# Performance work log

Measured on AMD Instinct MI355X. Metric: run time of the kernel, lower is better.

## Reference

```python
import jax, jax.numpy as jnp
import numpy as np

EPS = 1e-5


def _gcn_conv(x, src, dst, norm, W, b, n_nodes):
    # PyG GCNConv: transform, then normalized scatter-add aggregation (self-loops included in src/dst)
    h = x @ W                                   # [N, out]
    msg = h[src] * norm[:, None]                # gather over edges [E+N, out]
    agg = jax.ops.segment_sum(msg, dst, num_segments=n_nodes)
    return agg + b


def _bn(x, gamma, beta):
    # BatchNorm1d in training mode: batch stats over node axis, biased variance
    mu = jnp.mean(x, axis=0)
    var = jnp.mean((x - mu) ** 2, axis=0)
    return (x - mu) * jax.lax.rsqrt(var + EPS) * gamma + beta


def setup_inputs() -> dict:
    key = jax.random.key(0)
    ks = jax.random.split(key, 8)
    N, E, F_in, H, F_out = 50000, 800000, 32, 96, 2
    x = jax.random.normal(ks[0], (N, F_in), dtype=jnp.float32)
    edge_index = jax.random.randint(ks[1], (2, E), 0, N, dtype=jnp.int64)
    def lin(k, fi, fo):
        s = 1.0 / np.sqrt(fi)
        return jax.random.uniform(k, (fi, fo), jnp.float32, -s, s)
    W1 = lin(ks[2], F_in, H); b1 = jnp.zeros((H,), jnp.float32)
    W2 = lin(ks[3], H, H);    b2 = jnp.zeros((H,), jnp.float32)
    W3 = lin(ks[4], H, H);    b3 = jnp.zeros((H,), jnp.float32)
    W4 = lin(ks[5], H, F_out); b4 = jnp.zeros((F_out,), jnp.float32)
    g1 = jnp.ones((H,), jnp.float32); be1 = jnp.zeros((H,), jnp.float32)
    g2 = jnp.ones((H,), jnp.float32); be2 = jnp.zeros((H,), jnp.float32)
    g3 = jnp.ones((H,), jnp.float32); be3 = jnp.zeros((H,), jnp.float32)
    return dict(x=x, edge_index=edge_index,
                W1=W1, b1=b1, g1=g1, be1=be1,
                W2=W2, b2=b2, g2=g2, be2=be2,
                W3=W3, b3=b3, g3=g3, be3=be3,
                W4=W4, b4=b4)


def reference(x, edge_index, W1, b1, g1, be1, W2, b2, g2, be2, W3, b3, g3, be3, W4, b4):
    N = x.shape[0]
    loop = jnp.arange(N, dtype=edge_index.dtype)
    src = jnp.concatenate([edge_index[0], loop])   # add self-loops
    dst = jnp.concatenate([edge_index[1], loop])
    deg = jax.ops.segment_sum(jnp.ones_like(dst, dtype=x.dtype), dst, num_segments=N)
    dinv = jnp.where(deg > 0, jax.lax.rsqrt(deg), 0.0)
    norm = dinv[src] * dinv[dst]                   # D^{-1/2} (A+I) D^{-1/2}

    h = jax.nn.relu(_bn(_gcn_conv(x, src, dst, norm, W1, b1, N), g1, be1))
    h = jax.nn.relu(_bn(_gcn_conv(h, src, dst, norm, W2, b2, N), g2, be2))
    h = jax.nn.relu(_bn(_gcn_conv(h, src, dst, norm, W3, b3, N), g3, be3))
    return _gcn_conv(h, src, dst, norm, W4, b4, N)
```

## Files before the change

kernel.cpp:

```cpp
#include <hip/hip_runtime.h>
#include <hip/hip_bf16.h>

using bf16x8 = __attribute__((ext_vector_type(8))) short;
using f32x4  = __attribute__((ext_vector_type(4))) float;

__device__ __forceinline__ float ldf(const void* p, size_t i, float isf){
  if (isf > 0.5f) return ((const float*)p)[i];
  unsigned int u = ((unsigned int)((const unsigned short*)p)[i]) << 16;
  return __uint_as_float(u);
}
__device__ __forceinline__ unsigned short f2bf(float v){
  unsigned int u = __float_as_uint(v);
  u = (u + 0x7FFFu + ((u >> 16) & 1u)) >> 16;
  return (unsigned short)u;
}
__device__ __forceinline__ unsigned int pk2(float a, float b){
  return (unsigned int)f2bf(a) | ((unsigned int)f2bf(b) << 16);
}
__device__ __forceinline__ float lo16(unsigned int u){ return __uint_as_float(u << 16); }
__device__ __forceinline__ float hi16(unsigned int u){ return __uint_as_float(u & 0xFFFF0000u); }

__global__ void k_fill(unsigned short* o, unsigned short v, int n){
  int i = blockIdx.x*blockDim.x + threadIdx.x;
  if (i < n) o[i] = v;
}

__global__ void k_prep(const unsigned short* xh, const unsigned int* eu,
                       float* flag, int nelemX, long long E,
                       const void* W1, const void* W2, const void* W3, const void* W4,
                       unsigned short* __restrict__ Wt1, unsigned short* __restrict__ Wt2,
                       unsigned short* __restrict__ Wt3, float* __restrict__ W4f,
                       int* __restrict__ cnt, float* __restrict__ stAll, int n){
  int t = threadIdx.x;
  if (blockIdx.x > 0){
    int total = n + 4609;
    for (int i = (int)(blockIdx.x-1)*256 + t; i < total; i += (int)(gridDim.x-1)*256){
      if (i < n) cnt[i] = 0; else stAll[i - n] = 0.f;
    }
    return;
  }
  __shared__ int sf32, si64;
  __shared__ float sisf;
  if (t == 0){ sf32 = 0; si64 = 1; }
  __syncthreads();
  {
    int i = 2*t;
    if (i < nelemX){
      unsigned e8 = (xh[i] >> 7) & 0xFFu;
      if (e8 >= 140u) sf32 = 1;
    }
    if ((long long)(2*t + 1) < 2*E){
      if (eu[2*t + 1] != 0u) si64 = 0;
    }
  }
  __syncthreads();
  if (t == 0){
    flag[0] = (float)sf32; flag[1] = (float)si64;
    sisf = (float)sf32;
  }
  __syncthreads();
  float isf = sisf;
  for (int q = t; q < 3072; q += 256){
    int nn = q >> 5, k = q & 31;
    Wt1[q] = f2bf(ldf(W1, (size_t)96*k + nn, isf));
  }
  for (int q = t; q < 9216; q += 256){
    int nn = q/96, k = q - 96*nn;
    Wt2[q] = f2bf(ldf(W2, (size_t)96*k + nn, isf));
    Wt3[q] = f2bf(ldf(W3, (size_t)96*k + nn, isf));
  }
  if (t < 192) W4f[t] = ldf(W4, t, isf);
}

__global__ void k_cnt(const int* __restrict__ ei, const float* __restrict__ flag,
                      int* __restrict__ cnt, long long E, int n){
  long long i = (long long)blockIdx.x*blockDim.x + threadIdx.x;
  if (i >= E) return;
  int d = (flag[1] > 0.5f) ? ei[2*E + 2*i] : ei[E + i];
  if ((unsigned)d < (unsigned)n) atomicAdd(&cnt[d], 1);
}

__global__ void k_emit2(const int* __restrict__ cnt, int* __restrict__ gctr,
                        int* __restrict__ rowst, int* __restrict__ cursor,
                        float* __restrict__ dinv, int n){
  int i = blockIdx.x*256 + threadIdx.x;
  int lane = threadIdx.x & 63;
  int v = (i < n) ? cnt[i] : 0;
  int s = v;
  #pragma unroll
  for (int off = 1; off < 64; off <<= 1){
    int u = __shfl_up(s, off, 64);
    if (lane >= off) s += u;
  }
  int wtot = __shfl(s, 63, 64);
  int base = 0;
  if (lane == 63) base = atomicAdd(gctr, wtot);
  base = __shfl(base, 63, 64);
  if (i < n){
    int r = base + s - v;
    rowst[i]  = r;
    cursor[i] = r;
    dinv[i]   = rsqrtf((float)(1 + v));
  }
}

#define FS_CHUNK 4096
template<typename IT>
__global__ __launch_bounds__(256) void k_fl1(const int* __restrict__ ei,
      const float* __restrict__ flag, int* __restrict__ cursor, IT* __restrict__ csr,
      long long E, int n, int gF8,
      const void* __restrict__ x, const unsigned short* __restrict__ Wt1b,
      const float* __restrict__ dinv, unsigned short* __restrict__ HS){
  __shared__ __align__(16) unsigned short Xs[64][40];
  __shared__ __align__(16) unsigned short Wt[96][40];
  int t = threadIdx.x;
  if ((int)blockIdx.x < gF8){
    int part = blockIdx.x & 7;
    long long base = (long long)(blockIdx.x >> 3) * FS_CHUNK;
    int pl = (int)(((long long)n *  part     ) >> 3);
    int pr = (int)(((long long)n * (part + 1)) >> 3);
    bool i64 = (flag[1] > 0.5f);
    long long lim = base + FS_CHUNK < E ? base + FS_CHUNK : E;
    for (long long i = base + t; i < lim; i += 256){
      int s, d;
      if (i64){ s = ei[2*i]; d = ei[2*E + 2*i]; }
      else    { s = ei[i];   d = ei[E + i];     }
      if (d >= pl && d < pr && (unsigned)s < (unsigned)n){
        int p = atomicAdd(&cursor[d], 1);
        csr[p] = (IT)s;
      }
    }
    return;
  }
  int bid = blockIdx.x - gF8;
  float isf = flag[0];
  for (int q = t; q < 384; q += 256){
    uint4 v = ((const uint4*)Wt1b)[q];
    *(uint4*)&Wt[q >> 2][(q & 3)*8] = v;
  }
  {
    int row = t >> 2, part = t & 3;
    int node = bid*64 + row;
    uint4 o;
    if (node < n){
      if (isf > 0.5f){
        const float* xr = (const float*)x + (size_t)32*node + 8*part;
        o.x = pk2(xr[0], xr[1]); o.y = pk2(xr[2], xr[3]);
        o.z = pk2(xr[4], xr[5]); o.w = pk2(xr[6], xr[7]);
      } else {
        o = ((const uint4*)x)[(size_t)4*node + part];
      }
    } else { o.x = o.y = o.z = o.w = 0u; }
    *(uint4*)&Xs[row][8*part] = o;
  }
  __syncthreads();

  int wv = t >> 6, lane = t & 63;
  int m = lane & 15, quad = lane >> 4;
  bf16x8 av = *(const bf16x8*)&Xs[16*wv + m][8*quad];
  f32x4 acc[6];
  #pragma unroll
  for (int c = 0; c < 6; ++c) acc[c] = (f32x4)(0.f);
  #pragma unroll
  for (int c = 0; c < 6; ++c){
    bf16x8 bv = *(const bf16x8*)&Wt[16*c + m][8*quad];
    acc[c] = __builtin_amdgcn_mfma_f32_16x16x32_bf16(av, bv, acc[c], 0, 0, 0);
  }
  int rowbase = bid*64 + 16*wv + 4*quad;
  float div[4];
  #pragma unroll
  for (int r = 0; r < 4; ++r){ int rr = rowbase + r; div[r] = (rr < n) ? dinv[rr] : 0.f; }
  #pragma unroll
  for (int c = 0; c < 6; ++c){
    int col = 16*c + m;
    #pragma unroll
    for (int r = 0; r < 4; ++r){
      int rr = rowbase + r;
      if (rr < n) HS[(size_t)96*rr + col] = f2bf(acc[c][r]*div[r]);
    }
  }
}

#define ACC8(v) { a0+=lo16((v).x); a1+=hi16((v).x); a2+=lo16((v).y); a3+=hi16((v).y); \
                  a4+=lo16((v).z); a5+=hi16((v).z); a6+=lo16((v).w); a7+=hi16((v).w); }
template<typename IT>
__global__ __launch_bounds__(192) void k_agg(const uint4* __restrict__ hsr,
      const int* __restrict__ rowst, const int* __restrict__ cnt,
      const IT* __restrict__ csr,
      const float* __restrict__ dinv, uint4* __restrict__ zb4,
      float* __restrict__ stout, int n){
  __shared__ float ls[16][97], lq[16][97];
  int g = threadIdx.x, ty = threadIdx.y;
  int t = ty*12 + g;
  int node = blockIdx.x*16 + ty;
  float r[8];
  if (node < n){
    uint4 v = hsr[(size_t)node*12 + g];
    float a0 = lo16(v.x), a1 = hi16(v.x), a2 = lo16(v.y), a3 = hi16(v.y);
    float a4 = lo16(v.z), a5 = hi16(v.z), a6 = lo16(v.w), a7 = hi16(v.w);
    int b = rowst[node], e = b + cnt[node];
    int j = b;
    for (; j + 7 < e; j += 8){
      uint4 v0 = hsr[(size_t)csr[j]  *12 + g];
      uint4 v1 = hsr[(size_t)csr[j+1]*12 + g];
      uint4 v2 = hsr[(size_t)csr[j+2]*12 + g];
      uint4 v3 = hsr[(size_t)csr[j+3]*12 + g];
      uint4 v4 = hsr[(size_t)csr[j+4]*12 + g];
      uint4 v5 = hsr[(size_t)csr[j+5]*12 + g];
      uint4 v6 = hsr[(size_t)csr[j+6]*12 + g];
      uint4 v7 = hsr[(size_t)csr[j+7]*12 + g];
      ACC8(v0); ACC8(v1); ACC8(v2); ACC8(v3);
      ACC8(v4); ACC8(v5); ACC8(v6); ACC8(v7);
    }
    for (; j + 3 < e; j += 4){
      uint4 v0 = hsr[(size_t)csr[j]  *12 + g];
      uint4 v1 = hsr[(size_t)csr[j+1]*12 + g];
      uint4 v2 = hsr[(size_t)csr[j+2]*12 + g];
      uint4 v3 = hsr[(size_t)csr[j+3]*12 + g];
      ACC8(v0); ACC8(v1); ACC8(v2); ACC8(v3);
    }
    for (; j < e; ++j){
      uint4 vv = hsr[(size_t)csr[j]*12 + g];
      ACC8(vv);
    }
    float di = dinv[node];
    uint4 o;
    o.x = pk2(a0*di, a1*di);
    o.y = pk2(a2*di, a3*di);
    o.z = pk2(a4*di, a5*di);
    o.w = pk2(a6*di, a7*di);
    zb4[(size_t)node*12 + g] = o;
    r[0]=lo16(o.x); r[1]=hi16(o.x); r[2]=lo16(o.y); r[3]=hi16(o.y);
    r[4]=lo16(o.z); r[5]=hi16(o.z); r[6]=lo16(o.w); r[7]=hi16(o.w);
  } else {
    #pragma unroll
    for (int jj = 0; jj < 8; ++jj) r[jj] = 0.f;
  }
  #pragma unroll
  for (int jj = 0; jj < 8; ++jj){
    ls[ty][8*g + jj] = r[jj];
    lq[ty][8*g + jj] = r[jj]*r[jj];
  }
  __syncthreads();
  if (t < 96){
    float s = 0.f, q = 0.f;
    #pragma unroll
    for (int rr = 0; rr < 16; ++rr){ s += ls[rr][t]; q += lq[rr][t]; }
    int rep = blockIdx.x & 7;
    atomicAdd(&stout[192*rep + t],      s);
    atomicAdd(&stout[192*rep + 96 + t], q);
  }
}

__global__ __launch_bounds__(256) void k_linm(const unsigned short* __restrict__ zb,
      const unsigned short* __restrict__ Wtb, const float* __restrict__ st,
      const void* __restrict__ gam, const void* __restrict__ bet,
      const float* __restrict__ flag, const float* __restrict__ dinv,
      unsigned short* __restrict__ HS, int n, float invN){
  __shared__ float sa[96], sc[96];
  __shared__ __align__(16) unsigned short Ys[64][104];
  __shared__ __align__(16) unsigned short Wt[96][104];
  int t = threadIdx.x;
  if (t < 96){
    float ssum = 0.f, qsum = 0.f;
    #pragma unroll
    for (int r = 0; r < 8; ++r){ ssum += st[192*r + t]; qsum += st[192*r + 96 + t]; }
    float isf = flag[0];
    float mu  = ssum*invN;
    float var = fmaxf(qsum*invN - mu*mu, 0.f);
    float istd = rsqrtf(var + 1e-5f);
    float a = ldf(gam, t, isf)*istd;
    sa[t] = a; sc[t] = ldf(bet, t, isf) - mu*a;
  }
  for (int q = t; q < 1152; q += 256){
    uint4 v = ((const uint4*)Wtb)[q];
    *(uint4*)&Wt[q/12][8*(q - 12*(q/12))] = v;
  }
  __syncthreads();
  {
    int row = t >> 2, part = t & 3;
    int node = blockIdx.x*64 + row;
    if (node < n){
      const uint4* zr = (const uint4*)(zb + (size_t)96*node) + 3*part;
      #pragma unroll
      for (int q = 0; q < 3; ++q){
        uint4 zz = zr[q];
        int k = 24*part + 8*q;
        float y0 = fmaxf(lo16(zz.x)*sa[k]   + sc[k],   0.f);
        float y1 = fmaxf(hi16(zz.x)*sa[k+1] + sc[k+1], 0.f);
        float y2 = fmaxf(lo16(zz.y)*sa[k+2] + sc[k+2], 0.f);
        float y3 = fmaxf(hi16(zz.y)*sa[k+3] + sc[k+3], 0.f);
        float y4 = fmaxf(lo16(zz.z)*sa[k+4] + sc[k+4], 0.f);
        float y5 = fmaxf(hi16(zz.z)*sa[k+5] + sc[k+5], 0.f);
        float y6 = fmaxf(lo16(zz.w)*sa[k+6] + sc[k+6], 0.f);
        float y7 = fmaxf(hi16(zz.w)*sa[k+7] + sc[k+7], 0.f);
        *(unsigned int*)&Ys[row][k]     = pk2(y0, y1);
        *(unsigned int*)&Ys[row][k + 2] = pk2(y2, y3);
        *(unsigned int*)&Ys[row][k + 4] = pk2(y4, y5);
        *(unsigned int*)&Ys[row][k + 6] = pk2(y6, y7);
      }
    } else {
      unsigned int* yp = (unsigned int*)&Ys[row][24*part];
      #pragma unroll
      for (int q = 0; q < 12; ++q) yp[q] = 0u;
    }
  }
  __syncthreads();

  int wv = t >> 6, lane = t & 63;
  int m = lane & 15, quad = lane >> 4;
  bf16x8 av[3];
  #pragma unroll
  for (int kt = 0; kt < 3; ++kt)
    av[kt] = *(const bf16x8*)&Ys[16*wv + m][32*kt + 8*quad];
  f32x4 acc[6];
  #pragma unroll
  for (int c = 0; c < 6; ++c) acc[c] = (f32x4)(0.f);
  #pragma unroll
  for (int c = 0; c < 6; ++c){
    const unsigned short* wrow = &Wt[16*c + m][8*quad];
    #pragma unroll
    for (int kt = 0; kt < 3; ++kt){
      bf16x8 bv = *(const bf16x8*)(wrow + 32*kt);
      acc[c] = __builtin_amdgcn_mfma_f32_16x16x32_bf16(av[kt], bv, acc[c], 0, 0, 0);
    }
  }
  int rowbase = blockIdx.x*64 + 16*wv + 4*quad;
  float div[4];
  #pragma unroll
  for (int r = 0; r < 4; ++r){ int rr = rowbase + r; div[r] = (rr < n) ? dinv[rr] : 0.f; }
  #pragma unroll
  for (int c = 0; c < 6; ++c){
    int col = 16*c + m;
    #pragma unroll
    for (int r = 0; r < 4; ++r){
      int rr = rowbase + r;
      if (rr < n) HS[(size_t)96*rr + col] = f2bf(acc[c][r]*div[r]);
    }
  }
}

__global__ __launch_bounds__(256) void k_lin4(const unsigned short* __restrict__ zb,
      const float* __restrict__ Wf, const float* __restrict__ st,
      const void* __restrict__ gam, const void* __restrict__ bet,
      const float* __restrict__ flag, const float* __restrict__ dinv,
      float* __restrict__ hs2, int n, float invN){
  __shared__ float sa[96], sc[96];
  int t = threadIdx.x;
  if (t < 96){
    float ssum = 0.f, qsum = 0.f;
    #pragma unroll
    for (int r = 0; r < 8; ++r){ ssum += st[192*r + t]; qsum += st[192*r + 96 + t]; }
    float isf = flag[0];
    float mu  = ssum*invN;
    float var = fmaxf(qsum*invN - mu*mu, 0.f);
    float istd = rsqrtf(var + 1e-5f);
    float a = ldf(gam, t, isf)*istd;
    sa[t] = a; sc[t] = ldf(bet, t, isf) - mu*a;
  }
  __syncthreads();
  int i = blockIdx.x*blockDim.x + t;
  if (i >= n) return;
  const uint4* zr = (const uint4*)(zb + (size_t)96*i);
  float a0 = 0.f, a1 = 0.f;
  #pragma unroll
  for (int q = 0; q < 12; ++q){
    uint4 zz = zr[q];
    int k = 8*q;
    float y;
    y = fmaxf(lo16(zz.x)*sa[k]   + sc[k],   0.f); a0 += y*Wf[2*k];    a1 += y*Wf[2*k+1];
    y = fmaxf(hi16(zz.x)*sa[k+1] + sc[k+1], 0.f); a0 += y*Wf[2*k+2];  a1 += y*Wf[2*k+3];
    y = fmaxf(lo16(zz.y)*sa[k+2] + sc[k+2], 0.f); a0 += y*Wf[2*k+4];  a1 += y*Wf[2*k+5];
    y = fmaxf(hi16(zz.y)*sa[k+3] + sc[k+3], 0.f); a0 += y*Wf[2*k+6];  a1 += y*Wf[2*k+7];
    y = fmaxf(lo16(zz.z)*sa[k+4] + sc[k+4], 0.f); a0 += y*Wf[2*k+8];  a1 += y*Wf[2*k+9];
    y = fmaxf(hi16(zz.z)*sa[k+5] + sc[k+5], 0.f); a0 += y*Wf[2*k+10]; a1 += y*Wf[2*k+11];
    y = fmaxf(lo16(zz.w)*sa[k+6] + sc[k+6], 0.f); a0 += y*Wf[2*k+12]; a1 += y*Wf[2*k+13];
    y = fmaxf(hi16(zz.w)*sa[k+7] + sc[k+7], 0.f); a0 += y*Wf[2*k+14]; a1 += y*Wf[2*k+15];
  }
  float di = dinv[i];
  hs2[(size_t)2*i]   = di*a0;
  hs2[(size_t)2*i+1] = di*a1;
}

template<typename IT>
__global__ void k_agg2(const float2* __restrict__ hs2, const int* __restrict__ rowst,
                       const int* __restrict__ cnt, const IT* __restrict__ csr,
                       const float* __restrict__ dinv,
                       const void* __restrict__ b4, const float* __restrict__ flag,
                       void* __restrict__ out, int n){
  int node = blockIdx.x*blockDim.x + threadIdx.x;
  if (node >= n) return;
  float2 a = hs2[node];
  int b = rowst[node], e = b + cnt[node];
  for (int j = b; j < e; ++j){
    float2 v = hs2[(size_t)csr[j]];
    a.x += v.x; a.y += v.y;
  }
  float isf = flag[0];
  float di = dinv[node];
  float v0 = a.x*di + ldf(b4, 0, isf);
  float v1 = a.y*di + ldf(b4, 1, isf);
  if (isf > 0.5f){
    ((float*)out)[(size_t)2*node]   = v0;
    ((float*)out)[(size_t)2*node+1] = v1;
  } else {
    ((unsigned short*)out)[(size_t)2*node]   = f2bf(v0);
    ((unsigned short*)out)[(size_t)2*node+1] = f2bf(v1);
  }
}

extern "C" void kernel_launch(void* const* d_in, const int* in_sizes, int n_in,
                              void* d_out, int out_size, void* d_ws, size_t ws_size,
                              hipStream_t stream)
{
  const int B = 256;
  unsigned short* outh = (unsigned short*)d_out;

  if (n_in < 16){
    k_fill<<<(out_size+B-1)/B, B, 0, stream>>>(outh, 0x3F40u, out_size); return;
  }
  const int N = in_sizes[0] / 32;
  const long long E = in_sizes[1] / 2;
  if (in_sizes[0] % 32 != 0 || out_size != 2*N){
    k_fill<<<(out_size+B-1)/B, B, 0, stream>>>(outh, 0x3F60u, out_size); return;
  }
  const bool u16 = (N < 65536);

  size_t Npad = ((size_t)N + 3) & ~(size_t)3;
  float* ws   = (float*)d_ws;
  float* dinv = ws;
  float* hs2  = dinv + Npad;
  float* flag = hs2 + (size_t)2*N;
  float* stAll= flag + 4;
  float* W4f  = stAll + 4612;
  unsigned short* Wt1b = (unsigned short*)(W4f + 192);
  unsigned short* Wt2b = Wt1b + 3072;
  unsigned short* Wt3b = Wt2b + 9216;
  int* cnt    = (int*)(Wt3b + 9216);
  int* cursor = cnt + N;
  int* rowst  = cursor + N;
  void* csrv  = (void*)(rowst + N);
  size_t csrBytes = (size_t)E * (u16 ? 2 : 4);
  uintptr_t hp_ = (uintptr_t)csrv + csrBytes;
  hp_ = (hp_ + 15) & ~(uintptr_t)15;
  unsigned short* HS = (unsigned short*)hp_;
  unsigned short* Zb = HS + (size_t)96*N;

  size_t needB = ((uintptr_t)(Zb + (size_t)96*N) - (uintptr_t)d_ws) + 64;
  if (ws_size < needB){
    k_fill<<<(out_size+B-1)/B, B, 0, stream>>>(outh, 0x3F00u, out_size); return;
  }

  const void* x  = d_in[0];
  const int*  ei = (const int*)d_in[1];
  const void* W1 = d_in[2];
  const void* g1 = d_in[4];  const void* be1 = d_in[5];
  const void* W2 = d_in[6];
  const void* g2 = d_in[8];  const void* be2 = d_in[9];
  const void* W3 = d_in[10];
  const void* g3 = d_in[12]; const void* be3 = d_in[13];
  const void* W4 = d_in[14];
  const void* b4 = d_in[15];

  float* stA = stAll;
  float* stB = stAll + 1536;
  float* stC = stAll + 3072;
  int*   gctr = (int*)(stAll + 4608);

  int gN  = (N + B - 1)/B;
  int gE  = (int)((E + B - 1)/B);
  int nb  = (N + 255)/256;
  int gA  = (N + 15)/16;
  int gL  = (N + 63)/64;
  int gF8 = (int)((E + FS_CHUNK - 1)/FS_CHUNK) * 8;
  float invN = 1.0f / (float)N;
  dim3 ablk(12,16);

  k_prep<<<33, B, 0, stream>>>((const unsigned short*)x, (const unsigned int*)ei,
                               flag, in_sizes[0], E, W1, W2, W3, W4,
                               Wt1b, Wt2b, Wt3b, W4f, cnt, stAll, N);
  k_cnt<<<gE, B, 0, stream>>>(ei, flag, cnt, E, N);
  k_emit2<<<nb, B, 0, stream>>>(cnt, gctr, rowst, cursor, dinv, N);

  if (u16){
    unsigned short* csr = (unsigned short*)csrv;
    k_fl1<unsigned short><<<gF8 + gL, B, 0, stream>>>(ei, flag, cursor, csr, E, N, gF8,
                                                      x, Wt1b, dinv, HS);
    k_agg<unsigned short><<<gA, ablk, 0, stream>>>((const uint4*)HS, rowst, cnt, csr, dinv, (uint4*)Zb, stA, N);
    k_linm<<<gL, B, 0, stream>>>(Zb, Wt2b, stA, g1, be1, flag, dinv, HS, N, invN);
    k_agg<unsigned short><<<gA, ablk, 0, stream>>>((const uint4*)HS, rowst, cnt, csr, dinv, (uint4*)Zb, stB, N);
    k_linm<<<gL, B, 0, stream>>>(Zb, Wt3b, stB, g2, be2, flag, dinv, HS, N, invN);
    k_agg<unsigned short><<<gA, ablk, 0, stream>>>((const uint4*)HS, rowst, cnt, csr, dinv, (uint4*)Zb, stC, N);
    k_lin4<<<gN, B, 0, stream>>>(Zb, W4f, stC, g3, be3, flag, dinv, hs2, N, invN);
    k_agg2<unsigned short><<<gN, B, 0, stream>>>((const float2*)hs2, rowst, cnt, csr, dinv, b4, flag, d_out, N);
  } else {
    int* csr = (int*)csrv;
    k_fl1<int><<<gF8 + gL, B, 0, stream>>>(ei, flag, cursor, csr, E, N, gF8,
                                           x, Wt1b, dinv, HS);
    k_agg<int><<<gA, ablk, 0, stream>>>((const uint4*)HS, rowst, cnt, csr, dinv, (uint4*)Zb, stA, N);
    k_linm<<<gL, B, 0, stream>>>(Zb, Wt2b, stA, g1, be1, flag, dinv, HS, N, invN);
    k_agg<int><<<gA, ablk, 0, stream>>>((const uint4*)HS, rowst, cnt, csr, dinv, (uint4*)Zb, stB, N);
    k_linm<<<gL, B, 0, stream>>>(Zb, Wt3b, stB, g2, be2, flag, dinv, HS, N, invN);
    k_agg<int><<<gA, ablk, 0, stream>>>((const uint4*)HS, rowst, cnt, csr, dinv, (uint4*)Zb, stC, N);
    k_lin4<<<gN, B, 0, stream>>>(Zb, W4f, stC, g3, be3, flag, dinv, hs2, N, invN);
    k_agg2<int><<<gN, B, 0, stream>>>((const float2*)hs2, rowst, cnt, csr, dinv, b4, flag, d_out, N);
  }
}
```

Measured before the change: 340.8 us.

## Fuse whole GCN pipeline into one persistent cooperative kernel with grid syncs

Replaces the chain of about eleven kernel launches with a single cooperative persistent kernel. The grid is sized by occupancy, and grid.sync() separates the prep, degree count, scan, CSR fill, aggregation, linear and final stages. Each stage becomes a grid-stride loop over the old block indices, and shared memory is a union of the per-stage layouts. The goal is to remove per-launch overhead and inter-kernel gaps. In exchange, occupancy is limited by the largest shared-memory stage, and the aggregation stage now runs 192 of 256 threads per block. A host-side device-properties and occupancy query is added on every call, and the old multi-kernel path remains as a fallback.

```diff
diff --git a/kernel.cpp b/kernel.cpp
--- a/kernel.cpp
+++ b/kernel.cpp
@@ -1,8 +1,13 @@
 #include <hip/hip_runtime.h>
 #include <hip/hip_bf16.h>
+#include <hip/hip_cooperative_groups.h>
+
+namespace cg = cooperative_groups;
 
 using bf16x8 = __attribute__((ext_vector_type(8))) short;
 using f32x4  = __attribute__((ext_vector_type(4))) float;
+
+#define FS_CHUNK 4096
 
 __device__ __forceinline__ float ldf(const void* p, size_t i, float isf){
   if (isf > 0.5f) return ((const float*)p)[i];
@@ -23,6 +28,411 @@
 __global__ void k_fill(unsigned short* o, unsigned short v, int n){
   int i = blockIdx.x*blockDim.x + threadIdx.x;
   if (i < n) o[i] = v;
+}
+
+struct SLin1 { unsigned short Xs[64][40]; unsigned short Wt[96][40]; };
+struct SLinm { float sa[96]; float sc[96]; unsigned short Ys[64][104]; unsigned short Wt[96][104]; };
+struct SAgg  { float ls[16][97]; float lq[16][97]; };
+union __align__(16) SMem { SLin1 l1; SLinm lm; SAgg ag; };
+
+struct KParams {
+  const int* ei;
+  const void* x;
+  const void *W1, *W2, *W3, *W4;
+  const void *g1, *be1, *g2, *be2, *g3, *be3, *b4;
+  float* flag; float* stAll; float* W4f;
+  unsigned short *Wt1, *Wt2, *Wt3;
+  int *cnt, *cursor, *rowst;
+  void* csrv;
+  float *dinv, *hs2;
+  unsigned short *HS, *Zb;
+  void* out;
+  long long E;
+  int n, nelemX, gF8, gL, gA, gN;
+  float invN;
+};
+
+#define ACC8(v) { a0+=lo16((v).x); a1+=hi16((v).x); a2+=lo16((v).y); a3+=hi16((v).y); \
+                  a4+=lo16((v).z); a5+=hi16((v).z); a6+=lo16((v).w); a7+=hi16((v).w); }
+
+template<typename IT>
+__device__ void agg_stage(const KParams& p, SMem& sm, const IT* csr, float* stout, int t, int nbk){
+  const uint4* hsr = (const uint4*)p.HS;
+  uint4* zb4 = (uint4*)p.Zb;
+  int g = t % 12, ty = t / 12;
+  for (int va = blockIdx.x; va < p.gA; va += nbk){
+    float r[8];
+    if (t < 192){
+      int node = va*16 + ty;
+      if (node < p.n){
+        uint4 v = hsr[(size_t)node*12 + g];
+        float a0 = lo16(v.x), a1 = hi16(v.x), a2 = lo16(v.y), a3 = hi16(v.y);
+        float a4 = lo16(v.z), a5 = hi16(v.z), a6 = lo16(v.w), a7 = hi16(v.w);
+        int b = p.rowst[node], e = b + p.cnt[node];
+        int j = b;
+        for (; j + 7 < e; j += 8){
+          uint4 v0 = hsr[(size_t)csr[j]  *12 + g];
+          uint4 v1 = hsr[(size_t)csr[j+1]*12 + g];
+          uint4 v2 = hsr[(size_t)csr[j+2]*12 + g];
+          uint4 v3 = hsr[(size_t)csr[j+3]*12 + g];
+          uint4 v4 = hsr[(size_t)csr[j+4]*12 + g];
+          uint4 v5 = hsr[(size_t)csr[j+5]*12 + g];
+          uint4 v6 = hsr[(size_t)csr[j+6]*12 + g];
+          uint4 v7 = hsr[(size_t)csr[j+7]*12 + g];
+          ACC8(v0); ACC8(v1); ACC8(v2); ACC8(v3);
+          ACC8(v4); ACC8(v5); ACC8(v6); ACC8(v7);
+        }
+        for (; j + 3 < e; j += 4){
+          uint4 v0 = hsr[(size_t)csr[j]  *12 + g];
+          uint4 v1 = hsr[(size_t)csr[j+1]*12 + g];
+          uint4 v2 = hsr[(size_t)csr[j+2]*12 + g];
+          uint4 v3 = hsr[(size_t)csr[j+3]*12 + g];
+          ACC8(v0); ACC8(v1); ACC8(v2); ACC8(v3);
+        }
+        for (; j < e; ++j){
+          uint4 vv = hsr[(size_t)csr[j]*12 + g];
+          ACC8(vv);
+        }
+        float di = p.dinv[node];
+        uint4 o;
+        o.x = pk2(a0*di, a1*di);
+        o.y = pk2(a2*di, a3*di);
+        o.z = pk2(a4*di, a5*di);
+        o.w = pk2(a6*di, a7*di);
+        zb4[(size_t)node*12 + g] = o;
+        r[0]=lo16(o.x); r[1]=hi16(o.x); r[2]=lo16(o.y); r[3]=hi16(o.y);
+        r[4]=lo16(o.z); r[5]=hi16(o.z); r[6]=lo16(o.w); r[7]=hi16(o.w);
+      } else {
+        #pragma unroll
+        for (int jj = 0; jj < 8; ++jj) r[jj] = 0.f;
+      }
+      #pragma unroll
+      for (int jj = 0; jj < 8; ++jj){
+        sm.ag.ls[ty][8*g + jj] = r[jj];
+        sm.ag.lq[ty][8*g + jj] = r[jj]*r[jj];
+      }
+    }
+    __syncthreads();
+    if (t < 96){
+      float s = 0.f, q = 0.f;
+      #pragma unroll
+      for (int rr = 0; rr < 16; ++rr){ s += sm.ag.ls[rr][t]; q += sm.ag.lq[rr][t]; }
+      int rep = va & 7;
+      atomicAdd(&stout[192*rep + t],      s);
+      atomicAdd(&stout[192*rep + 96 + t], q);
+    }
+    __syncthreads();
+  }
+}
+
+__device__ void linm_stage(const KParams& p, SMem& sm, const unsigned short* Wtb,
+                           const float* st, const void* gam, const void* bet,
+                           int t, int nbk, float isf){
+  if (t < 96){
+    float ssum = 0.f, qsum = 0.f;
+    #pragma unroll
+    for (int r = 0; r < 8; ++r){ ssum += st[192*r + t]; qsum += st[192*r + 96 + t]; }
+    float mu  = ssum*p.invN;
+    float var = fmaxf(qsum*p.invN - mu*mu, 0.f);
+    float istd = rsqrtf(var + 1e-5f);
+    float a = ldf(gam, t, isf)*istd;
+    sm.lm.sa[t] = a; sm.lm.sc[t] = ldf(bet, t, isf) - mu*a;
+  }
+  for (int q = t; q < 1152; q += 256){
+    uint4 v = ((const uint4*)Wtb)[q];
+    *(uint4*)&sm.lm.Wt[q/12][8*(q - 12*(q/12))] = v;
+  }
+  __syncthreads();
+  int lane = t & 63, wv = t >> 6;
+  for (int vb = blockIdx.x; vb < p.gL; vb += nbk){
+    {
+      int row = t >> 2, part = t & 3;
+      int node = vb*64 + row;
+      if (node < p.n){
+        const uint4* zr = (const uint4*)(p.Zb + (size_t)96*node) + 3*part;
+        #pragma unroll
+        for (int q = 0; q < 3; ++q){
+          uint4 zz = zr[q];
+          int k = 24*part + 8*q;
+          float y0 = fmaxf(lo16(zz.x)*sm.lm.sa[k]   + sm.lm.sc[k],   0.f);
+          float y1 = fmaxf(hi16(zz.x)*sm.lm.sa[k+1] + sm.lm.sc[k+1], 0.f);
+          float y2 = fmaxf(lo16(zz.y)*sm.lm.sa[k+2] + sm.lm.sc[k+2], 0.f);
+          float y3 = fmaxf(hi16(zz.y)*sm.lm.sa[k+3] + sm.lm.sc[k+3], 0.f);
+          float y4 = fmaxf(lo16(zz.z)*sm.lm.sa[k+4] + sm.lm.sc[k+4], 0.f);
+          float y5 = fmaxf(hi16(zz.z)*sm.lm.sa[k+5] + sm.lm.sc[k+5], 0.f);
+          float y6 = fmaxf(lo16(zz.w)*sm.lm.sa[k+6] + sm.lm.sc[k+6], 0.f);
+          float y7 = fmaxf(hi16(zz.w)*sm.lm.sa[k+7] + sm.lm.sc[k+7], 0.f);
+          *(unsigned int*)&sm.lm.Ys[row][k]     = pk2(y0, y1);
+          *(unsigned int*)&sm.lm.Ys[row][k + 2] = pk2(y2, y3);
+          *(unsigned int*)&sm.lm.Ys[row][k + 4] = pk2(y4, y5);
+          *(unsigned int*)&sm.lm.Ys[row][k + 6] = pk2(y6, y7);
+        }
+      } else {
+        unsigned int* yp = (unsigned int*)&sm.lm.Ys[row][24*part];
+        #pragma unroll
+        for (int q = 0; q < 12; ++q) yp[q] = 0u;
+      }
+    }
+    __syncthreads();
+    int m = lane & 15, quad = lane >> 4;
+    bf16x8 av[3];
+    #pragma unroll
+    for (int kt = 0; kt < 3; ++kt)
+      av[kt] = *(const bf16x8*)&sm.lm.Ys[16*wv + m][32*kt + 8*quad];
+    f32x4 acc[6];
+    #pragma unroll
+    for (int c = 0; c < 6; ++c) acc[c] = (f32x4)(0.f);
+    #pragma unroll
+    for (int c = 0; c < 6; ++c){
+      const unsigned short* wrow = &sm.lm.Wt[16*c + m][8*quad];
+      #pragma unroll
+      for (int kt = 0; kt < 3; ++kt){
+        bf16x8 bv = *(const bf16x8*)(wrow + 32*kt);
+        acc[c] = __builtin_amdgcn_mfma_f32_16x16x32_bf16(av[kt], bv, acc[c], 0, 0, 0);
+      }
+    }
+    int rowbase = vb*64 + 16*wv + 4*quad;
+    float div[4];
+    #pragma unroll
+    for (int r = 0; r < 4; ++r){ int rr = rowbase + r; div[r] = (rr < p.n) ? p.dinv[rr] : 0.f; }
+    #pragma unroll
+    for (int c = 0; c < 6; ++c){
+      int col = 16*c + m;
+      #pragma unroll
+      for (int r = 0; r < 4; ++r){
+        int rr = rowbase + r;
+        if (rr < p.n) p.HS[(size_t)96*rr + col] = f2bf(acc[c][r]*div[r]);
+      }
+    }
+    __syncthreads();
+  }
+}
+
+template<typename IT>
+__global__ __launch_bounds__(256) void k_mega(KParams p){
+  cg::grid_group grid = cg::this_grid();
+  __shared__ SMem sm;
+  __shared__ int sflags[2];
+  const int t = threadIdx.x;
+  const int nbk = (int)gridDim.x;
+  const int lane = t & 63, wv = t >> 6;
+  IT* csr = (IT*)p.csrv;
+  int* gctr = (int*)(p.stAll + 4608);
+  float* stA = p.stAll;
+  float* stB = p.stAll + 1536;
+  float* stC = p.stAll + 3072;
+
+  if (blockIdx.x == 0){
+    if (t == 0){ sflags[0] = 0; sflags[1] = 1; }
+    __syncthreads();
+    {
+      int i = 2*t;
+      if (i < p.nelemX){
+        unsigned e8 = (((const unsigned short*)p.x)[i] >> 7) & 0xFFu;
+        if (e8 >= 140u) sflags[0] = 1;
+      }
+      if ((long long)(2*t+1) < 2*p.E){
+        if (((const unsigned int*)p.ei)[2*t+1] != 0u) sflags[1] = 0;
+      }
+    }
+    __syncthreads();
+    if (t == 0){ p.flag[0] = (float)sflags[0]; p.flag[1] = (float)sflags[1]; }
+    float isf0 = (float)sflags[0];
+    for (int q = t; q < 3072; q += 256){
+      int nn = q >> 5, k = q & 31;
+      p.Wt1[q] = f2bf(ldf(p.W1, (size_t)96*k + nn, isf0));
+    }
+    for (int q = t; q < 9216; q += 256){
+      int nn = q/96, k = q - 96*nn;
+      p.Wt2[q] = f2bf(ldf(p.W2, (size_t)96*k + nn, isf0));
+      p.Wt3[q] = f2bf(ldf(p.W3, (size_t)96*k + nn, isf0));
+    }
+    if (t < 192) p.W4f[t] = ldf(p.W4, t, isf0);
+  } else {
+    int total = p.n + 4609;
+    for (int i = (int)(blockIdx.x-1)*256 + t; i < total; i += (nbk-1)*256){
+      if (i < p.n) p.cnt[i] = 0; else p.stAll[i - p.n] = 0.f;
+    }
+  }
+  __threadfence();
+  grid.sync();
+
+  const bool i64 = p.flag[1] > 0.5f;
+  const float isf = p.flag[0];
+
+  for (long long i = (long long)blockIdx.x*256 + t; i < p.E; i += (long long)nbk*256){
+    int d = i64 ? p.ei[2*p.E + 2*i] : p.ei[p.E + i];
+    if ((unsigned)d < (unsigned)p.n) atomicAdd(&p.cnt[d], 1);
+  }
+  __threadfence();
+  grid.sync();
+
+  {
+    int chunks = (p.n + 255) >> 8;
+    for (int c = blockIdx.x; c < chunks; c += nbk){
+      int i = c*256 + t;
+      int v = (i < p.n) ? p.cnt[i] : 0;
+      int s = v;
+      #pragma unroll
+      for (int off = 1; off < 64; off <<= 1){
+        int u = __shfl_up(s, off, 64);
+        if (lane >= off) s += u;
+      }
+      int wtot = __shfl(s, 63, 64);
+      int base = 0;
+      if (lane == 63) base = atomicAdd(gctr, wtot);
+      base = __shfl(base, 63, 64);
+      if (i < p.n){
+        int r = base + s - v;
+        p.rowst[i]  = r;
+        p.cursor[i] = r;
+        p.dinv[i]   = rsqrtf((float)(1 + v));
+      }
+    }
+  }
+  __threadfence();
+  grid.sync();
+
+  for (int q = t; q < 384; q += 256){
+    uint4 v = ((const uint4*)p.Wt1)[q];
+    *(uint4*)&sm.l1.Wt[q >> 2][(q & 3)*8] = v;
+  }
+  __syncthreads();
+  for (int vb = blockIdx.x; vb < p.gF8 + p.gL; vb += nbk){
+    if (vb < p.gF8){
+      int part = vb & 7;
+      long long base = (long long)(vb >> 3) * FS_CHUNK;
+      int pl = (int)(((long long)p.n *  part     ) >> 3);
+      int pr = (int)(((long long)p.n * (part + 1)) >> 3);
+      long long lim = base + FS_CHUNK < p.E ? base + FS_CHUNK : p.E;
+      for (long long i = base + t; i < lim; i += 256){
+        int s, d;
+        if (i64){ s = p.ei[2*i]; d = p.ei[2*p.E + 2*i]; }
+        else    { s = p.ei[i];   d = p.ei[p.E + i];     }
+        if (d >= pl && d < pr && (unsigned)s < (unsigned)p.n){
+          int pp = atomicAdd(&p.cursor[d], 1);
+          csr[pp] = (IT)s;
+        }
+      }
+    } else {
+      int bid = vb - p.gF8;
+      {
+        int row = t >> 2, part4 = t & 3;
+        int node = bid*64 + row;
+        uint4 o;
+        if (node < p.n){
+          if (isf > 0.5f){
+            const float* xr = (const float*)p.x + (size_t)32*node + 8*part4;
+            o.x = pk2(xr[0], xr[1]); o.y = pk2(xr[2], xr[3]);
+            o.z = pk2(xr[4], xr[5]); o.w = pk2(xr[6], xr[7]);
+          } else {
+            o = ((const uint4*)p.x)[(size_t)4*node + part4];
+          }
+        } else { o.x = o.y = o.z = o.w = 0u; }
+        *(uint4*)&sm.l1.Xs[row][8*part4] = o;
+      }
+      __syncthreads();
+      int m = lane & 15, quad = lane >> 4;
+      bf16x8 av = *(const bf16x8*)&sm.l1.Xs[16*wv + m][8*quad];
+      f32x4 acc[6];
+      #pragma unroll
+      for (int c = 0; c < 6; ++c) acc[c] = (f32x4)(0.f);
+      #pragma unroll
+      for (int c = 0; c < 6; ++c){
+        bf16x8 bv = *(const bf16x8*)&sm.l1.Wt[16*c + m][8*quad];
+        acc[c] = __builtin_amdgcn_mfma_f32_16x16x32_bf16(av, bv, acc[c], 0, 0, 0);
+      }
+      int rowbase = bid*64 + 16*wv + 4*quad;
+      float div[4];
+      #pragma unroll
+      for (int r = 0; r < 4; ++r){ int rr = rowbase + r; div[r] = (rr < p.n) ? p.dinv[rr] : 0.f; }
+      #pragma unroll
+      for (int c = 0; c < 6; ++c){
+        int col = 16*c + m;
+        #pragma unroll
+        for (int r = 0; r < 4; ++r){
+          int rr = rowbase + r;
+          if (rr < p.n) p.HS[(size_t)96*rr + col] = f2bf(acc[c][r]*div[r]);
+        }
+      }
+      __syncthreads();
+    }
+  }
+  __threadfence();
+  grid.sync();
+
+  agg_stage<IT>(p, sm, csr, stA, t, nbk);
+  __threadfence(); grid.sync();
+  linm_stage(p, sm, p.Wt2, stA, p.g1, p.be1, t, nbk, isf);
+  __threadfence(); grid.sync();
+  agg_stage<IT>(p, sm, csr, stB, t, nbk);
+  __threadfence(); grid.sync();
+  linm_stage(p, sm, p.Wt3, stB, p.g2, p.be2, t, nbk, isf);
+  __threadfence(); grid.sync();
+  agg_stage<IT>(p, sm, csr, stC, t, nbk);
+  __threadfence(); grid.sync();
+
+  if (t < 96){
+    float ssum = 0.f, qsum = 0.f;
+    #pragma unroll
+    for (int r = 0; r < 8; ++r){ ssum += stC[192*r + t]; qsum += stC[192*r + 96 + t]; }
+    float mu  = ssum*p.invN;
+    float var = fmaxf(qsum*p.invN - mu*mu, 0.f);
+    float istd = rsqrtf(var + 1e-5f);
+    float a = ldf(p.g3, t, isf)*istd;
+    sm.lm.sa[t] = a; sm.lm.sc[t] = ldf(p.be3, t, isf) - mu*a;
+  }
+  __syncthreads();
+  for (int vb = blockIdx.x; vb < p.gN; vb += nbk){
+    int i = vb*256 + t;
+    if (i < p.n){
+      const uint4* zr = (const uint4*)(p.Zb + (size_t)96*i);
+      float a0 = 0.f, a1 = 0.f;
+      #pragma unroll
+      for (int q = 0; q < 12; ++q){
+        uint4 zz = zr[q];
+        int k = 8*q;
+        const float* Wf = p.W4f;
+        float y;
+        y = fmaxf(lo16(zz.x)*sm.lm.sa[k]   + sm.lm.sc[k],   0.f); a0 += y*Wf[2*k];    a1 += y*Wf[2*k+1];
+        y = fmaxf(hi16(zz.x)*sm.lm.sa[k+1] + sm.lm.sc[k+1], 0.f); a0 += y*Wf[2*k+2];  a1 += y*Wf[2*k+3];
+        y = fmaxf(lo16(zz.y)*sm.lm.sa[k+2] + sm.lm.sc[k+2], 0.f); a0 += y*Wf[2*k+4];  a1 += y*Wf[2*k+5];
+        y = fmaxf(hi16(zz.y)*sm.lm.sa[k+3] + sm.lm.sc[k+3], 0.f); a0 += y*Wf[2*k+6];  a1 += y*Wf[2*k+7];
+        y = fmaxf(lo16(zz.z)*sm.lm.sa[k+4] + sm.lm.sc[k+4], 0.f); a0 += y*Wf[2*k+8];  a1 += y*Wf[2*k+9];
+        y = fmaxf(hi16(zz.z)*sm.lm.sa[k+5] + sm.lm.sc[k+5], 0.f); a0 += y*Wf[2*k+10]; a1 += y*Wf[2*k+11];
+        y = fmaxf(lo16(zz.w)*sm.lm.sa[k+6] + sm.lm.sc[k+6], 0.f); a0 += y*Wf[2*k+12]; a1 += y*Wf[2*k+13];
+        y = fmaxf(hi16(zz.w)*sm.lm.sa[k+7] + sm.lm.sc[k+7], 0.f); a0 += y*Wf[2*k+14]; a1 += y*Wf[2*k+15];
+      }
+      float di = p.dinv[i];
+      p.hs2[(size_t)2*i]   = di*a0;
+      p.hs2[(size_t)2*i+1] = di*a1;
+    }
+  }
+  __threadfence();
+  grid.sync();
+
+  for (int vb = blockIdx.x; vb < p.gN; vb += nbk){
+    int node = vb*256 + t;
+    if (node < p.n){
+      const float2* hs2 = (const float2*)p.hs2;
+      float2 a = hs2[node];
+      int b = p.rowst[node], e = b + p.cnt[node];
+      for (int j = b; j < e; ++j){
+        float2 v = hs2[(size_t)csr[j]];
+        a.x += v.x; a.y += v.y;
+      }
+      float di = p.dinv[node];
+      float v0 = a.x*di + ldf(p.b4, 0, isf);
+      float v1 = a.y*di + ldf(p.b4, 1, isf);
+      if (isf > 0.5f){
+        ((float*)p.out)[(size_t)2*node]   = v0;
+        ((float*)p.out)[(size_t)2*node+1] = v1;
+      } else {
+        ((unsigned short*)p.out)[(size_t)2*node]   = f2bf(v0);
+        ((unsigned short*)p.out)[(size_t)2*node+1] = f2bf(v1);
+      }
+    }
+  }
 }
 
 __global__ void k_prep(const unsigned short* xh, const unsigned int* eu,
@@ -54,10 +464,7 @@
     }
   }
   __syncthreads();
-  if (t == 0){
-    flag[0] = (float)sf32; flag[1] = (float)si64;
-    sisf = (float)sf32;
-  }
+  if (t == 0){ flag[0] = (float)sf32; flag[1] = (float)si64; sisf = (float)sf32; }
   __syncthreads();
   float isf = sisf;
   for (int q = t; q < 3072; q += 256){
@@ -104,7 +511,6 @@
   }
 }
 
-#define FS_CHUNK 4096
 template<typename IT>
 __global__ __launch_bounds__(256) void k_fl1(const int* __restrict__ ei,
       const float* __restrict__ flag, int* __restrict__ cursor, IT* __restrict__ csr,
@@ -154,7 +560,6 @@
     *(uint4*)&Xs[row][8*part] = o;
   }
   __syncthreads();
-
   int wv = t >> 6, lane = t & 63;
   int m = lane & 15, quad = lane >> 4;
   bf16x8 av = *(const bf16x8*)&Xs[16*wv + m][8*quad];
@@ -181,8 +586,6 @@
   }
 }
 
-#define ACC8(v) { a0+=lo16((v).x); a1+=hi16((v).x); a2+=lo16((v).y); a3+=hi16((v).y); \
-                  a4+=lo16((v).z); a5+=hi16((v).z); a6+=lo16((v).w); a7+=hi16((v).w); }
 template<typename IT>
 __global__ __launch_bounds__(192) void k_agg(const uint4* __restrict__ hsr,
       const int* __restrict__ rowst, const int* __restrict__ cnt,
@@ -306,7 +709,6 @@
     }
   }
   __syncthreads();
-
   int wv = t >> 6, lane = t & 63;
   int m = lane & 15, quad = lane >> 4;
   bf16x8 av[3];
@@ -462,11 +864,6 @@
   const void* W4 = d_in[14];
   const void* b4 = d_in[15];
 
-  float* stA = stAll;
-  float* stB = stAll + 1536;
-  float* stC = stAll + 3072;
-  int*   gctr = (int*)(stAll + 4608);
-
   int gN  = (N + B - 1)/B;
   int gE  = (int)((E + B - 1)/B);
   int nb  = (N + 255)/256;
@@ -474,18 +871,47 @@
   int gL  = (N + 63)/64;
   int gF8 = (int)((E + FS_CHUNK - 1)/FS_CHUNK) * 8;
   float invN = 1.0f / (float)N;
+
+  KParams kp;
+  kp.ei = ei; kp.x = x;
+  kp.W1 = W1; kp.W2 = W2; kp.W3 = W3; kp.W4 = W4;
+  kp.g1 = g1; kp.be1 = be1; kp.g2 = g2; kp.be2 = be2; kp.g3 = g3; kp.be3 = be3; kp.b4 = b4;
+  kp.flag = flag; kp.stAll = stAll; kp.W4f = W4f;
+  kp.Wt1 = Wt1b; kp.Wt2 = Wt2b; kp.Wt3 = Wt3b;
+  kp.cnt = cnt; kp.cursor = cursor; kp.rowst = rowst; kp.csrv = csrv;
+  kp.dinv = dinv; kp.hs2 = hs2; kp.HS = HS; kp.Zb = Zb; kp.out = d_out;
+  kp.E = E; kp.n = N; kp.nelemX = in_sizes[0];
+  kp.gF8 = gF8; kp.gL = gL; kp.gA = gA; kp.gN = gN;
+  kp.invN = invN;
+
+  const void* fn = u16 ? (const void*)k_mega<unsigned short> : (const void*)k_mega<int>;
+  int dev = 0; hipGetDevice(&dev);
+  hipDeviceProp_t prop;
+  hipError_t perr = hipGetDeviceProperties(&prop, dev);
+  int occ = 0;
+  hipError_t oerr = hipOccupancyMaxActiveBlocksPerMultiprocessor(&occ, fn, 256, 0);
+  hipError_t lerr = hipErrorUnknown;
+  if (perr == hipSuccess && oerr == hipSuccess && occ > 0){
+    int grid = prop.multiProcessorCount * occ;
+    if (grid < 8) grid = 8;
+    void* args[] = { (void*)&kp };
+    lerr = hipLaunchCooperativeKernel(fn, dim3(grid), dim3(256), args, 0, stream);
+  }
+  if (lerr == hipSuccess) return;
+
   dim3 ablk(12,16);
-
   k_prep<<<33, B, 0, stream>>>((const unsigned short*)x, (const unsigned int*)ei,
                                flag, in_sizes[0], E, W1, W2, W3, W4,
                                Wt1b, Wt2b, Wt3b, W4f, cnt, stAll, N);
   k_cnt<<<gE, B, 0, stream>>>(ei, flag, cnt, E, N);
+  int* gctr = (int*)(stAll + 4608);
   k_emit2<<<nb, B, 0, stream>>>(cnt, gctr, rowst, cursor, dinv, N);
-
+  float* stA = stAll;
+  float* stB = stAll + 1536;
+  float* stC = stAll + 3072;
   if (u16){
     unsigned short* csr = (unsigned short*)csrv;
-    k_fl1<unsigned short><<<gF8 + gL, B, 0, stream>>>(ei, flag, cursor, csr, E, N, gF8,
-                                                      x, Wt1b, dinv, HS);
+    k_fl1<unsigned short><<<gF8 + gL, B, 0, stream>>>(ei, flag, cursor, csr, E, N, gF8, x, Wt1b, dinv, HS);
     k_agg<unsigned short><<<gA, ablk, 0, stream>>>((const uint4*)HS, rowst, cnt, csr, dinv, (uint4*)Zb, stA, N);
     k_linm<<<gL, B, 0, stream>>>(Zb, Wt2b, stA, g1, be1, flag, dinv, HS, N, invN);
     k_agg<unsigned short><<<gA, ablk, 0, stream>>>((const uint4*)HS, rowst, cnt, csr, dinv, (uint4*)Zb, stB, N);
@@ -495,8 +921,7 @@
     k_agg2<unsigned short><<<gN, B, 0, stream>>>((const float2*)hs2, rowst, cnt, csr, dinv, b4, flag, d_out, N);
   } else {
     int* csr = (int*)csrv;
-    k_fl1<int><<<gF8 + gL, B, 0, stream>>>(ei, flag, cursor, csr, E, N, gF8,
-                                           x, Wt1b, dinv, HS);
+    k_fl1<int><<<gF8 + gL, B, 0, stream>>>(ei, flag, cursor, csr, E, N, gF8, x, Wt1b, dinv, HS);
     k_agg<int><<<gA, ablk, 0, stream>>>((const uint4*)HS, rowst, cnt, csr, dinv, (uint4*)Zb, stA, N);
     k_linm<<<gL, B, 0, stream>>>(Zb, Wt2b, stA, g1, be1, flag, dinv, HS, N, invN);
     k_agg<int><<<gA, ablk, 0, stream>>>((const uint4*)HS, rowst, cnt, csr, dinv, (uint4*)Zb, stB, N);
```

Measured after the change: 1.053 ms. 3.09x slower.
